# Optimization experiments

Hardware: AMD Instinct MI355X
Metric: run time of the kernel (lower is better)

## Reference

```python
import jax, jax.numpy as jnp
import numpy as np

NUM_RADIAL = 16
HIDDEN = 128
OUT_DIM = 128
N_LAYERS = 3
N_NODES = 20000
N_EDGES = 640000


def _orthogonal(key, rows, cols):
    # mimic nn.init.orthogonal_ for a [rows, cols] weight
    n = max(rows, cols)
    a = jax.random.normal(key, (n, min(rows, cols)), dtype=jnp.float32)
    q, r = jnp.linalg.qr(a)
    q = q * jnp.sign(jnp.diagonal(r))  # make deterministic-ish sign
    w = q[:rows, :cols] if rows >= cols else q[:cols, :rows].T
    return w.astype(jnp.float32)


def setup_inputs() -> dict:
    key = jax.random.key(0)
    ks = jax.random.split(key, 8)
    distance_representation = jax.random.normal(ks[0], (N_EDGES, NUM_RADIAL), dtype=jnp.float32)
    message = jax.random.normal(ks[1], (N_EDGES, HIDDEN), dtype=jnp.float32)
    edge_index = jax.random.randint(ks[2], (2, N_EDGES), 0, N_NODES, dtype=jnp.int32)
    # parameters (torch Linear stores weight as [out, in])
    Wd = _orthogonal(ks[3], HIDDEN, NUM_RADIAL)          # linear_distance.weight
    layer_keys = jax.random.split(ks[4], N_LAYERS)
    Ws = jnp.stack([_orthogonal(k, HIDDEN, HIDDEN) for k in layer_keys])  # [L, H, H]
    bs = jnp.zeros((N_LAYERS, HIDDEN), dtype=jnp.float32)
    Wout = _orthogonal(ks[5], OUT_DIM, HIDDEN)           # linear_out.weight
    return {
        "distance_representation": distance_representation,
        "message": message,
        "edge_index": edge_index,
        "num_nodes": N_NODES,
        "Wd": Wd,
        "Ws": Ws,
        "bs": bs,
        "Wout": Wout,
    }


def reference(distance_representation, message, edge_index, num_nodes, Wd, Ws, bs, Wout):
    # distance gate: [E, NUM_RADIAL] @ Wd.T -> [E, H]
    gate = distance_representation @ Wd.T
    transformed_message = gate * message                 # [E, H]
    target_index = edge_index[1]
    # edge -> node scatter-add aggregation
    node_embedding = jax.ops.segment_sum(
        transformed_message, target_index, num_segments=num_nodes)  # [N, H]
    for i in range(Ws.shape[0]):
        node_embedding = jax.nn.silu(node_embedding @ Ws[i].T + bs[i])
    return node_embedding @ Wout.T                       # [N, OUT_DIM]
```

## Files before the change

### kernel.cpp

```cpp
#include <hip/hip_runtime.h>

#define HID 128
#define NR  16
#define NLAYER 4
#define CHUNK 16
#define MAXN_LDS 20480

__device__ __forceinline__ float dot4f(float4 a, float4 b) {
    return a.x * b.x + a.y * b.y + a.z * b.z + a.w * b.w;
}

__global__ void hist_kernel(const int* __restrict__ eidx, int* __restrict__ hist, int E) {
    int i = (blockIdx.x * blockDim.x + threadIdx.x) * 4;
    if (i + 4 <= E) {
        int4 v = *(const int4*)(eidx + E + i);
        atomicAdd(&hist[v.x], 1);
        atomicAdd(&hist[v.y], 1);
        atomicAdd(&hist[v.z], 1);
        atomicAdd(&hist[v.w], 1);
    } else {
        for (; i < E; ++i) atomicAdd(&hist[eidx[E + i]], 1);
    }
}

__global__ __launch_bounds__(1024) void prep_kernel(const int* __restrict__ hist,
                                                    int* __restrict__ curs, int N,
                                                    const float* __restrict__ Ws,
                                                    const float* __restrict__ Wout,
                                                    float* __restrict__ WT) {
    const int tid = threadIdx.x;
    if (blockIdx.x > 0) {
        int idx = (blockIdx.x - 1) * 1024 + tid;
        if (idx < NLAYER * HID * HID) {
            int l = idx >> 14;
            int rem = idx & 16383;
            int h = rem >> 7, k = rem & 127;
            const float* src = (l < 3) ? (Ws + ((size_t)l << 14)) : Wout;
            WT[((size_t)l << 14) + (size_t)k * HID + h] = src[(size_t)h * HID + k];
        }
        return;
    }
    __shared__ int sh[MAXN_LDS];
    __shared__ int part[1024];
    const bool use_lds = (N <= MAXN_LDS);
    if (use_lds) {
        for (int i = tid; i < N; i += 1024) sh[i] = hist[i];
        __syncthreads();
    }
    const int per = (N + 1023) >> 10;
    const int base = tid * per;
    int s = 0;
    for (int i = 0; i < per; ++i) {
        int idx = base + i;
        if (idx < N) s += use_lds ? sh[idx] : hist[idx];
    }
    part[tid] = s;
    __syncthreads();
    for (int off = 1; off < 1024; off <<= 1) {
        int v = part[tid];
        int add = (tid >= off) ? part[tid - off] : 0;
        __syncthreads();
        part[tid] = v + add;
        __syncthreads();
    }
    int run = (tid > 0) ? part[tid - 1] : 0;
    for (int i = 0; i < per; ++i) {
        int idx = base + i;
        if (idx < N) {
            curs[idx] = run;
            run += use_lds ? sh[idx] : hist[idx];
        }
    }
}

__global__ void scatter_kernel(const int* __restrict__ eidx, int* __restrict__ curs,
                               int2* __restrict__ pairs, int E) {
    int i = (blockIdx.x * blockDim.x + threadIdx.x) * 4;
    if (i + 4 <= E) {
        int4 v = *(const int4*)(eidx + E + i);
        int p;
        p = atomicAdd(&curs[v.x], 1); pairs[p] = make_int2(i + 0, v.x);
        p = atomicAdd(&curs[v.y], 1); pairs[p] = make_int2(i + 1, v.y);
        p = atomicAdd(&curs[v.z], 1); pairs[p] = make_int2(i + 2, v.z);
        p = atomicAdd(&curs[v.w], 1); pairs[p] = make_int2(i + 3, v.w);
    } else {
        for (; i < E; ++i) {
            int t = eidx[E + i];
            int p = atomicAdd(&curs[t], 1);
            pairs[p] = make_int2(i, t);
        }
    }
}

__global__ __launch_bounds__(256, 4) void gather_kernel(
    const float* __restrict__ dist, const float* __restrict__ msg,
    const float* __restrict__ Wd, const int2* __restrict__ pairs,
    float* __restrict__ node_emb, int E)
{
    __shared__ float sdist[4][CHUNK * NR];

    const int tid  = threadIdx.x;
    const int lane = tid & 63;
    const int wv   = tid >> 6;
    const long base = ((long)blockIdx.x * 4 + wv) * CHUNK;
    if (base >= E) return;
    const int cnt = (E - base < CHUNK) ? (int)(E - base) : CHUNK;

    const int base_ch = (lane >> 1) << 2;
    const int kh      = (lane & 1) * 8;
    float4 wdh[4][2];
#pragma unroll
    for (int j = 0; j < 4; ++j) {
        wdh[j][0] = *(const float4*)(Wd + (size_t)(base_ch + j) * NR + kh);
        wdh[j][1] = *(const float4*)(Wd + (size_t)(base_ch + j) * NR + kh + 4);
    }

    int ids[CHUNK], tg[CHUNK];
    if (cnt == CHUNK) {
#pragma unroll
        for (int q = 0; q < CHUNK / 2; ++q) {
            int4 v = *(const int4*)(pairs + base + q * 2);
            ids[q*2+0] = v.x; tg[q*2+0] = v.y;
            ids[q*2+1] = v.z; tg[q*2+1] = v.w;
        }
    } else {
#pragma unroll
        for (int i = 0; i < CHUNK; ++i) {
            int2 v = (i < cnt) ? pairs[base + i] : make_int2(0, -1);
            ids[i] = v.x; tg[i] = v.y;
        }
    }

    float dv[CHUNK / 4];
#pragma unroll
    for (int g = 0; g < CHUNK / 4; ++g) {
        int e = ids[g * 4 + (lane >> 4)];
        dv[g] = dist[(size_t)e * NR + (lane & 15)];
    }

    float2 m[CHUNK];
#pragma unroll
    for (int i = 0; i < CHUNK; ++i)
        m[i] = *(const float2*)(msg + (size_t)ids[i] * HID + 2 * lane);

    float* sd = sdist[wv];
#pragma unroll
    for (int g = 0; g < CHUNK / 4; ++g)
        sd[g * 64 + lane] = dv[g];

    const bool odd = (lane & 1);
    float a0 = 0.f, a1 = 0.f;
#pragma unroll
    for (int i = 0; i < CHUNK; ++i) {
        if (i < cnt) {
            const float4* dr = (const float4*)(sd + i * NR + kh);
            float4 d0 = dr[0], d1 = dr[1];
            float p0 = dot4f(d0, wdh[0][0]) + dot4f(d1, wdh[0][1]);
            float p1 = dot4f(d0, wdh[1][0]) + dot4f(d1, wdh[1][1]);
            float p2 = dot4f(d0, wdh[2][0]) + dot4f(d1, wdh[2][1]);
            float p3 = dot4f(d0, wdh[3][0]) + dot4f(d1, wdh[3][1]);
            float s0 = odd ? p0 : p2;
            float s1 = odd ? p1 : p3;
            float r0 = __shfl_xor(s0, 1, 64);
            float r1 = __shfl_xor(s1, 1, 64);
            float g0 = (odd ? p2 : p0) + r0;
            float g1 = (odd ? p3 : p1) + r1;
            a0 += g0 * m[i].x;
            a1 += g1 * m[i].y;
            bool fl = (i == cnt - 1) || (tg[i + 1] != tg[i]);
            if (fl) {
                float* dst = node_emb + (size_t)tg[i] * HID + 2 * lane;
                unsafeAtomicAdd(dst,     a0);
                unsafeAtomicAdd(dst + 1, a1);
                a0 = 0.f; a1 = 0.f;
            }
        }
    }
}

__global__ __launch_bounds__(512) void mlp_kernel(
    float* __restrict__ data, const float* __restrict__ WT,
    const float* __restrict__ bs, int N)
{
    __shared__ float xa[64][132];

    const int tid = threadIdx.x;
    const int nb  = blockIdx.x * 64;
    const int hq  = tid & 31, h0 = hq * 4;
    const int nq  = tid >> 5, n0 = nq * 4;

    for (int i = tid; i < 64 * 32; i += 512) {
        int n = i >> 5, kq = i & 31;
        float4 v = make_float4(0.f, 0.f, 0.f, 0.f);
        if (nb + n < N) v = *(const float4*)(data + (size_t)(nb + n) * HID + kq * 4);
        *(float4*)(&xa[n][kq * 4]) = v;
    }
    __syncthreads();

    for (int l = 0; l < NLAYER; ++l) {
        const float* __restrict__ W = WT + ((size_t)l << 14);
        float acc[4][4];
        if (l < 3) {
            float b[4];
#pragma unroll
            for (int j = 0; j < 4; ++j) b[j] = bs[l * HID + h0 + j];
#pragma unroll
            for (int i = 0; i < 4; ++i)
#pragma unroll
                for (int j = 0; j < 4; ++j) acc[i][j] = b[j];
        } else {
#pragma unroll
            for (int i = 0; i < 4; ++i)
#pragma unroll
                for (int j = 0; j < 4; ++j) acc[i][j] = 0.f;
        }

        for (int k4 = 0; k4 < 32; ++k4) {
            float4 xv[4];
#pragma unroll
            for (int i = 0; i < 4; ++i) xv[i] = *(const float4*)(&xa[n0 + i][k4 * 4]);
            float4 wr[4];
#pragma unroll
            for (int kk = 0; kk < 4; ++kk)
                wr[kk] = *(const float4*)(W + (size_t)(k4 * 4 + kk) * HID + h0);
#pragma unroll
            for (int i = 0; i < 4; ++i) {
                acc[i][0] += xv[i].x * wr[0].x + xv[i].y * wr[1].x + xv[i].z * wr[2].x + xv[i].w * wr[3].x;
                acc[i][1] += xv[i].x * wr[0].y + xv[i].y * wr[1].y + xv[i].z * wr[2].y + xv[i].w * wr[3].y;
                acc[i][2] += xv[i].x * wr[0].z + xv[i].y * wr[1].z + xv[i].z * wr[2].z + xv[i].w * wr[3].z;
                acc[i][3] += xv[i].x * wr[0].w + xv[i].y * wr[1].w + xv[i].z * wr[2].w + xv[i].w * wr[3].w;
            }
        }
        __syncthreads();

        if (l < 3) {
#pragma unroll
            for (int i = 0; i < 4; ++i) {
                float4 y;
                y.x = acc[i][0] / (1.f + __expf(-acc[i][0]));
                y.y = acc[i][1] / (1.f + __expf(-acc[i][1]));
                y.z = acc[i][2] / (1.f + __expf(-acc[i][2]));
                y.w = acc[i][3] / (1.f + __expf(-acc[i][3]));
                *(float4*)(&xa[n0 + i][h0]) = y;
            }
            __syncthreads();
        } else {
#pragma unroll
            for (int i = 0; i < 4; ++i) {
                if (nb + n0 + i < N) {
                    float4 y = make_float4(acc[i][0], acc[i][1], acc[i][2], acc[i][3]);
                    *(float4*)(data + (size_t)(nb + n0 + i) * HID + h0) = y;
                }
            }
        }
    }
}

extern "C" void kernel_launch(void* const* d_in, const int* in_sizes, int n_in,
                              void* d_out, int out_size, void* d_ws, size_t ws_size,
                              hipStream_t stream) {
    const float* dist = (const float*)d_in[0];
    const float* msg  = (const float*)d_in[1];
    const int*   eidx = (const int*)d_in[2];
    const float* Wd   = (const float*)d_in[4];
    const float* Ws   = (const float*)d_in[5];
    const float* bs   = (const float*)d_in[6];
    const float* Wout = (const float*)d_in[7];
    float* out = (float*)d_out;

    const int E = in_sizes[1] / HID;
    const int N = out_size / HID;

    int*   hist   = (int*)d_ws;
    int*   curs   = hist + N;
    size_t pr_off = ((size_t)(2 * N) + 3) & ~(size_t)3;
    int2*  pairs  = (int2*)((int*)d_ws + pr_off);
    size_t wt_off = (pr_off + (size_t)2 * E + 3) & ~(size_t)3;
    float* WT     = (float*)d_ws + wt_off;

    hipMemsetAsync(hist, 0, (size_t)N * sizeof(int), stream);
    hipMemsetAsync(out, 0, (size_t)N * HID * sizeof(float), stream);

    const int qE = (E + 3) / 4;
    const int tblocks = (NLAYER * HID * HID + 1023) / 1024;
    hist_kernel   <<<(qE + 255) / 256, 256, 0, stream>>>(eidx, hist, E);
    prep_kernel   <<<1 + tblocks, 1024, 0, stream>>>(hist, curs, N, Ws, Wout, WT);
    scatter_kernel<<<(qE + 255) / 256, 256, 0, stream>>>(eidx, curs, pairs, E);

    const long waves = ((long)E + CHUNK - 1) / CHUNK;
    gather_kernel <<<(int)((waves + 3) / 4), 256, 0, stream>>>(dist, msg, Wd, pairs, out, E);
    mlp_kernel    <<<(N + 63) / 64, 512, 0, stream>>>(out, WT, bs, N);
}
```

Baseline: 290.8 us.

## Software-pipeline gather over persistent per-wave chunk ranges and shrink MLP blocks

Measured after the change: 522.5 us. 1.8x slower.

```diff
diff --git a/kernel.cpp b/kernel.cpp
--- a/kernel.cpp
+++ b/kernel.cpp
@@ -3,8 +3,12 @@
 #define HID 128
 #define NR  16
 #define NLAYER 4
-#define CHUNK 16
+#define CH  8
+#define NC  20
 #define MAXN_LDS 20480
+
+struct PairBlk { int ids[CH]; int tg[CH]; };
+struct MsgBlk  { float2 m[CH]; };
 
 __device__ __forceinline__ float dot4f(float4 a, float4 b) {
     return a.x * b.x + a.y * b.y + a.z * b.z + a.w * b.w;
@@ -92,68 +96,44 @@
     }
 }
 
-__global__ __launch_bounds__(256, 4) void gather_kernel(
-    const float* __restrict__ dist, const float* __restrict__ msg,
-    const float* __restrict__ Wd, const int2* __restrict__ pairs,
-    float* __restrict__ node_emb, int E)
-{
-    __shared__ float sdist[4][CHUNK * NR];
-
-    const int tid  = threadIdx.x;
-    const int lane = tid & 63;
-    const int wv   = tid >> 6;
-    const long base = ((long)blockIdx.x * 4 + wv) * CHUNK;
-    if (base >= E) return;
-    const int cnt = (E - base < CHUNK) ? (int)(E - base) : CHUNK;
-
-    const int base_ch = (lane >> 1) << 2;
-    const int kh      = (lane & 1) * 8;
-    float4 wdh[4][2];
-#pragma unroll
-    for (int j = 0; j < 4; ++j) {
-        wdh[j][0] = *(const float4*)(Wd + (size_t)(base_ch + j) * NR + kh);
-        wdh[j][1] = *(const float4*)(Wd + (size_t)(base_ch + j) * NR + kh + 4);
-    }
-
-    int ids[CHUNK], tg[CHUNK];
-    if (cnt == CHUNK) {
-#pragma unroll
-        for (int q = 0; q < CHUNK / 2; ++q) {
-            int4 v = *(const int4*)(pairs + base + q * 2);
-            ids[q*2+0] = v.x; tg[q*2+0] = v.y;
-            ids[q*2+1] = v.z; tg[q*2+1] = v.w;
+__device__ __forceinline__ void load_pairs(const int2* __restrict__ pairs,
+                                           long ebase, int evalid, PairBlk& P) {
+    if (evalid >= CH) {
+#pragma unroll
+        for (int q = 0; q < CH / 2; ++q) {
+            int4 v = *(const int4*)(pairs + ebase + q * 2);
+            P.ids[2*q]   = v.x; P.tg[2*q]   = v.y;
+            P.ids[2*q+1] = v.z; P.tg[2*q+1] = v.w;
         }
     } else {
 #pragma unroll
-        for (int i = 0; i < CHUNK; ++i) {
-            int2 v = (i < cnt) ? pairs[base + i] : make_int2(0, -1);
-            ids[i] = v.x; tg[i] = v.y;
-        }
-    }
-
-    float dv[CHUNK / 4];
-#pragma unroll
-    for (int g = 0; g < CHUNK / 4; ++g) {
-        int e = ids[g * 4 + (lane >> 4)];
-        dv[g] = dist[(size_t)e * NR + (lane & 15)];
-    }
-
-    float2 m[CHUNK];
-#pragma unroll
-    for (int i = 0; i < CHUNK; ++i)
-        m[i] = *(const float2*)(msg + (size_t)ids[i] * HID + 2 * lane);
-
-    float* sd = sdist[wv];
-#pragma unroll
-    for (int g = 0; g < CHUNK / 4; ++g)
-        sd[g * 64 + lane] = dv[g];
-
-    const bool odd = (lane & 1);
-    float a0 = 0.f, a1 = 0.f;
-#pragma unroll
-    for (int i = 0; i < CHUNK; ++i) {
-        if (i < cnt) {
-            const float4* dr = (const float4*)(sd + i * NR + kh);
+        for (int i = 0; i < CH; ++i) {
+            if (i < evalid) { int2 v = pairs[ebase + i]; P.ids[i] = v.x; P.tg[i] = v.y; }
+            else            { P.ids[i] = 0; P.tg[i] = -1; }
+        }
+    }
+}
+
+__device__ __forceinline__ void load_md(const float* __restrict__ msg,
+                                        const float* __restrict__ dist,
+                                        const PairBlk& P, int lane,
+                                        MsgBlk& M, float dv[CH / 4]) {
+#pragma unroll
+    for (int j = 0; j < CH; ++j)
+        M.m[j] = *(const float2*)(msg + (size_t)P.ids[j] * HID + 2 * lane);
+#pragma unroll
+    for (int g = 0; g < CH / 4; ++g)
+        dv[g] = dist[(size_t)P.ids[g * 4 + (lane >> 4)] * NR + (lane & 15)];
+}
+
+__device__ __forceinline__ void compute_chunk(const float* __restrict__ sd,
+        const MsgBlk& M, const PairBlk& P, int tgNext0,
+        const float4 wdh[4][2], int kh, bool odd, int lane,
+        float& a0, float& a1, float* __restrict__ node_emb) {
+#pragma unroll
+    for (int j = 0; j < CH; ++j) {
+        if (P.tg[j] >= 0) {
+            const float4* dr = (const float4*)(sd + j * NR + kh);
             float4 d0 = dr[0], d1 = dr[1];
             float p0 = dot4f(d0, wdh[0][0]) + dot4f(d1, wdh[0][1]);
             float p1 = dot4f(d0, wdh[1][0]) + dot4f(d1, wdh[1][1]);
@@ -165,11 +145,11 @@
             float r1 = __shfl_xor(s1, 1, 64);
             float g0 = (odd ? p2 : p0) + r0;
             float g1 = (odd ? p3 : p1) + r1;
-            a0 += g0 * m[i].x;
-            a1 += g1 * m[i].y;
-            bool fl = (i == cnt - 1) || (tg[i + 1] != tg[i]);
-            if (fl) {
-                float* dst = node_emb + (size_t)tg[i] * HID + 2 * lane;
+            a0 += g0 * M.m[j].x;
+            a1 += g1 * M.m[j].y;
+            int tn = (j < CH - 1) ? P.tg[j + 1] : tgNext0;
+            if (tn != P.tg[j]) {
+                float* dst = node_emb + (size_t)P.tg[j] * HID + 2 * lane;
                 unsafeAtomicAdd(dst,     a0);
                 unsafeAtomicAdd(dst + 1, a1);
                 a0 = 0.f; a1 = 0.f;
@@ -178,18 +158,72 @@
     }
 }
 
-__global__ __launch_bounds__(512) void mlp_kernel(
+__global__ __launch_bounds__(256, 4) void gather_kernel(
+    const float* __restrict__ dist, const float* __restrict__ msg,
+    const float* __restrict__ Wd, const int2* __restrict__ pairs,
+    float* __restrict__ node_emb, int E)
+{
+    __shared__ float sdist[4][CH * NR];
+
+    const int tid  = threadIdx.x;
+    const int lane = tid & 63;
+    const int wv   = tid >> 6;
+    const long w   = (long)blockIdx.x * 4 + wv;
+    const long nchunks = ((long)E + CH - 1) / CH;
+    const long c0  = w * NC;
+    if (c0 >= nchunks) return;
+    const int nc = (int)(((nchunks - c0) < NC) ? (nchunks - c0) : NC);
+
+    const int base_ch = (lane >> 1) << 2;
+    const int kh      = (lane & 1) * 8;
+    const bool odd    = lane & 1;
+    float4 wdh[4][2];
+#pragma unroll
+    for (int jj = 0; jj < 4; ++jj) {
+        wdh[jj][0] = *(const float4*)(Wd + (size_t)(base_ch + jj) * NR + kh);
+        wdh[jj][1] = *(const float4*)(Wd + (size_t)(base_ch + jj) * NR + kh + 4);
+    }
+    float* sd = sdist[wv];
+
+    PairBlk PA, PB;
+    MsgBlk  MA, MB;
+    float dvA[CH / 4], dvB[CH / 4];
+    float a0 = 0.f, a1 = 0.f;
+
+#define EVALID(k) (((k) >= nc) ? 0 : (int)((((long)E - (c0 + (k)) * CH) >= CH) ? CH : ((long)E - (c0 + (k)) * CH)))
+
+    load_pairs(pairs, c0 * CH, EVALID(0), PA);
+    load_md(msg, dist, PA, lane, MA, dvA);
+    load_pairs(pairs, (c0 + 1) * CH, EVALID(1), PB);
+
+    for (int k = 0; k < nc; k += 2) {
+        load_md(msg, dist, PB, lane, MB, dvB);
+#pragma unroll
+        for (int g = 0; g < CH / 4; ++g) sd[g * 64 + lane] = dvA[g];
+        compute_chunk(sd, MA, PA, PB.tg[0], wdh, kh, odd, lane, a0, a1, node_emb);
+        load_pairs(pairs, (c0 + k + 2) * CH, EVALID(k + 2), PA);
+
+        load_md(msg, dist, PA, lane, MA, dvA);
+#pragma unroll
+        for (int g = 0; g < CH / 4; ++g) sd[g * 64 + lane] = dvB[g];
+        compute_chunk(sd, MB, PB, PA.tg[0], wdh, kh, odd, lane, a0, a1, node_emb);
+        load_pairs(pairs, (c0 + k + 3) * CH, EVALID(k + 3), PB);
+    }
+#undef EVALID
+}
+
+__global__ __launch_bounds__(256) void mlp_kernel(
     float* __restrict__ data, const float* __restrict__ WT,
     const float* __restrict__ bs, int N)
 {
-    __shared__ float xa[64][132];
+    __shared__ float xa[32][132];
 
     const int tid = threadIdx.x;
-    const int nb  = blockIdx.x * 64;
+    const int nb  = blockIdx.x * 32;
     const int hq  = tid & 31, h0 = hq * 4;
     const int nq  = tid >> 5, n0 = nq * 4;
 
-    for (int i = tid; i < 64 * 32; i += 512) {
+    for (int i = tid; i < 32 * 32; i += 256) {
         int n = i >> 5, kq = i & 31;
         float4 v = make_float4(0.f, 0.f, 0.f, 0.f);
         if (nb + n < N) v = *(const float4*)(data + (size_t)(nb + n) * HID + kq * 4);
@@ -287,7 +321,8 @@
     prep_kernel   <<<1 + tblocks, 1024, 0, stream>>>(hist, curs, N, Ws, Wout, WT);
     scatter_kernel<<<(qE + 255) / 256, 256, 0, stream>>>(eidx, curs, pairs, E);
 
-    const long waves = ((long)E + CHUNK - 1) / CHUNK;
+    const long nchunks = ((long)E + CH - 1) / CH;
+    const long waves   = (nchunks + NC - 1) / NC;
     gather_kernel <<<(int)((waves + 3) / 4), 256, 0, stream>>>(dist, msg, Wd, pairs, out, E);
-    mlp_kernel    <<<(N + 63) / 64, 512, 0, stream>>>(out, WT, bs, N);
-}
+    mlp_kernel    <<<(N + 31) / 32, 256, 0, stream>>>(out, WT, bs, N);
+}
```
